# Kernel optimization log

Hardware: AMD Instinct MI355X
Metric: run time of the kernel (lower is better)

The kernel has to match this reference:

```python
import jax, jax.numpy as jnp
import numpy as np

N = 4096
FIN = 256
FOUT = 256
H = 1  # num_heads MUST be 1: edge projections reshape [N,N,H] -> (1,N,N)
NEG_MASK = -1000000.0
LRELU_SLOPE = 0.2
ESP = 1e-06
LN_EPS = 1e-05


def setup_inputs() -> dict:
    key = jax.random.key(0)
    ks = jax.random.split(key, 9)
    nodes_features = jax.random.normal(ks[0], (N, FIN), dtype=jnp.float32)
    degree_matrix = jax.random.normal(ks[1], (N, N), dtype=jnp.float32)
    edges_features_distance = jax.random.uniform(ks[2], (N, N), dtype=jnp.float32)
    edges_features_bond = jax.random.uniform(ks[3], (N, N), dtype=jnp.float32)
    # learned parameters (xavier-ish scale)
    proj_param = jax.random.normal(ks[4], (H, FIN, FOUT), dtype=jnp.float32) * (1.0 / np.sqrt(FIN))
    a_src = jax.random.normal(ks[5], (H, FOUT, 1), dtype=jnp.float32) * (1.0 / np.sqrt(FOUT))
    a_tgt = jax.random.normal(ks[6], (H, FOUT, 1), dtype=jnp.float32) * (1.0 / np.sqrt(FOUT))
    w_dist = jax.random.normal(ks[7], (H, 1), dtype=jnp.float32)  # nn.Linear(1, H).weight
    w_bond = jax.random.normal(ks[8], (H, 1), dtype=jnp.float32)
    return {
        "nodes_features": nodes_features,
        "degree_matrix": degree_matrix,
        "edges_features_distance": edges_features_distance,
        "edges_features_bond": edges_features_bond,
        "proj_param": proj_param,
        "a_src": a_src,
        "a_tgt": a_tgt,
        "w_dist": w_dist,
        "w_bond": w_bond,
        "cutoff": 0,
    }


def reference(nodes_features, degree_matrix, edges_features_distance,
              edges_features_bond, proj_param, a_src, a_tgt, w_dist, w_bond,
              cutoff=0):
    n = nodes_features.shape[0]
    h, fin, fout = proj_param.shape
    # connectivity mask: keep degree where positive, else large negative
    connectivity_mask = jnp.where(degree_matrix > 0, degree_matrix, NEG_MASK)
    # node projection: [H, N, Fout] (dropout is identity in eval)
    proj = jnp.einsum('nf,hfo->hno', nodes_features, proj_param)
    # attention scores: outer-sum of per-node source/target scores
    s_src = jnp.einsum('hno,hoi->hni', proj, a_src)      # [H, N, 1]
    s_tgt = jnp.einsum('hno,hoi->hni', proj, a_tgt)      # [H, N, 1]
    all_scores = jax.nn.leaky_relu(s_src + jnp.swapaxes(s_tgt, 1, 2), LRELU_SLOPE)  # [H,N,N]
    # edge contributions: Linear(1, H) on scalar edge features, reshaped (1,N,N) (H==1)
    dist_c = ((-edges_features_distance)[..., None] * w_dist[:, 0]).reshape(1, n, n)
    bond_c = (edges_features_bond[..., None] * w_bond[:, 0]).reshape(1, n, n)
    all_scores = all_scores + dist_c + bond_c
    # masked softmax over neighbors
    attn = jax.nn.softmax(all_scores + connectivity_mask[None], axis=-1)  # [H,N,N]
    # weighted aggregation
    out = jnp.einsum('hnm,hmo->hno', attn, proj)  # [H, N, Fout]
    # faithful to torch: transpose(2,1) -> [H,Fout,N] then contiguous view(-1,H,Fout)
    out = jnp.transpose(out, (0, 2, 1)).reshape(-1, h, fout)
    # concat heads (skip connection and bias are disabled per init args)
    out = out.reshape(-1, h * fout)
    out = jax.nn.elu(out)  # ELU activation, alpha=1
    # ---- no_grad connectivity update ----
    o = jax.lax.stop_gradient(out)
    dm = jax.lax.stop_gradient(degree_matrix)
    sim = o @ o.T                                        # [N, N]
    decay = -jax.lax.stop_gradient(edges_features_distance)
    upd = jax.nn.sigmoid(sim) * decay * (dm > 0).astype(o.dtype)
    upd = upd + ESP
    mean = jnp.mean(upd, axis=-1, keepdims=True)
    var = jnp.mean(jnp.square(upd - mean), axis=-1, keepdims=True)
    upd = (upd - mean) / jnp.sqrt(var + LN_EPS)          # layer_norm, no affine
    upd = upd + upd.T
    return out, upd
```

## Files before the change

### kernel.cpp

```cpp
#include <hip/hip_runtime.h>


using f32x4  = __attribute__((ext_vector_type(4))) float;
using bf16x8 = __attribute__((ext_vector_type(8))) __bf16;
using bf16x4 = __attribute__((ext_vector_type(4))) __bf16;
using u32x4  = __attribute__((ext_vector_type(4))) unsigned int;

__global__ __launch_bounds__(256) void cvt_nodes_kernel(const float* __restrict__ x,
                                                        __bf16* __restrict__ y) {
  int i = (blockIdx.x * 256 + threadIdx.x) * 4;
  f32x4 v = *(const f32x4*)(x + i);
  bf16x4 o = { (__bf16)v[0], (__bf16)v[1], (__bf16)v[2], (__bf16)v[3] };
  *(bf16x4*)(y + i) = o;
}

__global__ __launch_bounds__(256) void cvt_wt_kernel(const float* __restrict__ w,
                                                     __bf16* __restrict__ wt) {
  int i = blockIdx.x * 256 + threadIdx.x;
  int o = i >> 8, f = i & 255;
  wt[i] = (__bf16)w[f * 256 + o];
}

template<int BM, int BN, int MODE>
__global__ __launch_bounds__(256) void gemm_bf16_kernel(
    const __bf16* __restrict__ A, const __bf16* __restrict__ Bt,
    int M, int N, int K,
    float* __restrict__ outf, __bf16* __restrict__ outb,
    const float* __restrict__ e0, const float* __restrict__ e1,
    const __bf16* __restrict__ axp, float* __restrict__ outt)
{
  constexpr int LDT = 72;
  constexpr int MI = BM / 32;
  constexpr int NI = BN / 32;
  __shared__ alignas(16) __bf16 As[BM * LDT];
  __shared__ alignas(16) __bf16 Bs[BN * LDT];
  const int tid  = threadIdx.x;
  const int lane = tid & 63;
  const int wid  = tid >> 6;
  const int wm0  = (wid >> 1) * (BM / 2);
  const int wn0  = (wid & 1) * (BN / 2);
  const int m0   = blockIdx.x * BM;
  const int n0   = blockIdx.y * BN;
  const int lr   = lane & 15;
  const int lk   = lane >> 4;

  f32x4 acc[MI][NI];
#pragma unroll
  for (int a = 0; a < MI; ++a)
#pragma unroll
    for (int b = 0; b < NI; ++b) acc[a][b] = (f32x4){0.f, 0.f, 0.f, 0.f};

  for (int kt = 0; kt < K; kt += 64) {
    __syncthreads();
    for (int idx = tid; idx < BM * 8; idx += 256) {
      int r = idx >> 3, c = idx & 7;
      u32x4 v = *(const u32x4*)(A + (size_t)(m0 + r) * K + kt + c * 8);
      *(u32x4*)(As + r * LDT + c * 8) = v;
    }
    for (int idx = tid; idx < BN * 8; idx += 256) {
      int r = idx >> 3, c = idx & 7;
      u32x4 v = *(const u32x4*)(Bt + (size_t)(n0 + r) * K + kt + c * 8);
      *(u32x4*)(Bs + r * LDT + c * 8) = v;
    }
    __syncthreads();
#pragma unroll
    for (int kk = 0; kk < 2; ++kk) {
      bf16x8 av[MI], bv[NI];
#pragma unroll
      for (int mi = 0; mi < MI; ++mi)
        av[mi] = *(const bf16x8*)(As + (wm0 + mi * 16 + lr) * LDT + kk * 32 + lk * 8);
#pragma unroll
      for (int ni = 0; ni < NI; ++ni)
        bv[ni] = *(const bf16x8*)(Bs + (wn0 + ni * 16 + lr) * LDT + kk * 32 + lk * 8);
#pragma unroll
      for (int mi = 0; mi < MI; ++mi)
#pragma unroll
        for (int ni = 0; ni < NI; ++ni)
          acc[mi][ni] = __builtin_amdgcn_mfma_f32_16x16x32_bf16(av[mi], bv[ni], acc[mi][ni], 0, 0, 0);
    }
  }

#pragma unroll
  for (int mi = 0; mi < MI; ++mi) {
#pragma unroll
    for (int ni = 0; ni < NI; ++ni) {
#pragma unroll
      for (int j = 0; j < 4; ++j) {
        const int m = m0 + wm0 + mi * 16 + lk * 4 + j;
        const int n = n0 + wn0 + ni * 16 + lr;
        const float v = acc[mi][ni][j];
        if constexpr (MODE == 0) {
          outf[(size_t)m * 256 + n] = v;
          outb[(size_t)n * 4096 + m] = (__bf16)v;
        } else if constexpr (MODE == 2) {
          const size_t idx = (size_t)m * 4096 + n;
          const float d = e0[idx];
          const float g = e1[idx];
          const float s = 1.0f / (1.0f + expf(-v));
          outt[idx] = s * (-d) * (g > 0.f ? 1.0f : 0.0f) + 1e-6f;
        } else {
          const size_t idx = (size_t)m * 4096 + n;
          const float a = (float)axp[idx];
          const float s = 1.0f / (1.0f + expf(-v));
          outt[idx] = s * a + 1e-6f;
        }
      }
    }
  }
}

__global__ __launch_bounds__(256) void gemm_splitk_kernel(
    const __bf16* __restrict__ A, const __bf16* __restrict__ Bt,
    float* __restrict__ partial)
{
  constexpr int LDT = 72;
  __shared__ alignas(16) __bf16 As[64 * LDT];
  __shared__ alignas(16) __bf16 Bs[64 * LDT];
  const int tid  = threadIdx.x;
  const int lane = tid & 63;
  const int wid  = tid >> 6;
  const int wm0  = (wid >> 1) * 32;
  const int wn0  = (wid & 1) * 32;
  const int m0   = blockIdx.x * 64;
  const int n0   = blockIdx.y * 64;
  const int s    = blockIdx.z;
  const int lr   = lane & 15;
  const int lk   = lane >> 4;

  f32x4 acc[2][2];
#pragma unroll
  for (int a = 0; a < 2; ++a)
#pragma unroll
    for (int b = 0; b < 2; ++b) acc[a][b] = (f32x4){0.f, 0.f, 0.f, 0.f};

  const int k0 = s * 512;
  for (int kt = k0; kt < k0 + 512; kt += 64) {
    __syncthreads();
    for (int idx = tid; idx < 512; idx += 256) {
      int r = idx >> 3, c = idx & 7;
      u32x4 v = *(const u32x4*)(A + (size_t)(m0 + r) * 4096 + kt + c * 8);
      *(u32x4*)(As + r * LDT + c * 8) = v;
    }
    for (int idx = tid; idx < 512; idx += 256) {
      int r = idx >> 3, c = idx & 7;
      u32x4 v = *(const u32x4*)(Bt + (size_t)(n0 + r) * 4096 + kt + c * 8);
      *(u32x4*)(Bs + r * LDT + c * 8) = v;
    }
    __syncthreads();
#pragma unroll
    for (int kk = 0; kk < 2; ++kk) {
      bf16x8 av[2], bv[2];
#pragma unroll
      for (int mi = 0; mi < 2; ++mi)
        av[mi] = *(const bf16x8*)(As + (wm0 + mi * 16 + lr) * LDT + kk * 32 + lk * 8);
#pragma unroll
      for (int ni = 0; ni < 2; ++ni)
        bv[ni] = *(const bf16x8*)(Bs + (wn0 + ni * 16 + lr) * LDT + kk * 32 + lk * 8);
#pragma unroll
      for (int mi = 0; mi < 2; ++mi)
#pragma unroll
        for (int ni = 0; ni < 2; ++ni)
          acc[mi][ni] = __builtin_amdgcn_mfma_f32_16x16x32_bf16(av[mi], bv[ni], acc[mi][ni], 0, 0, 0);
    }
  }

  float* P = partial + (size_t)s * (4096 * 256);
#pragma unroll
  for (int mi = 0; mi < 2; ++mi)
#pragma unroll
    for (int ni = 0; ni < 2; ++ni)
#pragma unroll
      for (int j = 0; j < 4; ++j) {
        const int m = m0 + wm0 + mi * 16 + lk * 4 + j;
        const int n = n0 + wn0 + ni * 16 + lr;
        P[(size_t)m * 256 + n] = acc[mi][ni][j];
      }
}

__global__ __launch_bounds__(256) void reduce_elu_kernel(
    const float* __restrict__ partial, float* __restrict__ out0,
    __bf16* __restrict__ E)
{
  __shared__ float tile[64][65];
  const int tid = threadIdx.x;
  const int m0 = blockIdx.x * 64;
  const int n0 = blockIdx.y * 64;
#pragma unroll
  for (int i = 0; i < 4; ++i) {
    int lin = i * 1024 + tid * 4;
    int r = lin >> 6, c = lin & 63;
    f32x4 sum = (f32x4){0.f, 0.f, 0.f, 0.f};
#pragma unroll
    for (int s = 0; s < 8; ++s)
      sum += *(const f32x4*)(partial + (size_t)s * (4096 * 256) +
                             (size_t)(m0 + r) * 256 + n0 + c);
    tile[r][c]     = sum[0];
    tile[r][c + 1] = sum[1];
    tile[r][c + 2] = sum[2];
    tile[r][c + 3] = sum[3];
  }
  __syncthreads();
#pragma unroll
  for (int i = 0; i < 4; ++i) {
    int lin = i * 1024 + tid * 4;
    int rr = lin >> 6, cc = lin & 63;
    f32x4 e;
#pragma unroll
    for (int q = 0; q < 4; ++q) {
      float v = tile[cc + q][rr];
      e[q] = v > 0.f ? v : expm1f(v);
    }
    size_t idx = (size_t)(n0 + rr) * 4096 + m0 + cc;
    *(f32x4*)(out0 + idx) = e;
    bf16x4 eb = { (__bf16)e[0], (__bf16)e[1], (__bf16)e[2], (__bf16)e[3] };
    *(bf16x4*)(E + idx) = eb;
  }
}

__global__ __launch_bounds__(256) void sproj_kernel(const float* __restrict__ proj,
                                                    const float* __restrict__ asrc,
                                                    const float* __restrict__ atgt,
                                                    float* __restrict__ ssrc,
                                                    float* __restrict__ stgt) {
  const int row  = blockIdx.x * 4 + (threadIdx.x >> 6);
  const int lane = threadIdx.x & 63;
  f32x4 p = *(const f32x4*)(proj + (size_t)row * 256 + lane * 4);
  f32x4 a = *(const f32x4*)(asrc + lane * 4);
  f32x4 b = *(const f32x4*)(atgt + lane * 4);
  float d1 = p[0]*a[0] + p[1]*a[1] + p[2]*a[2] + p[3]*a[3];
  float d2 = p[0]*b[0] + p[1]*b[1] + p[2]*b[2] + p[3]*b[3];
#pragma unroll
  for (int o = 32; o; o >>= 1) { d1 += __shfl_xor(d1, o, 64); d2 += __shfl_xor(d2, o, 64); }
  if (lane == 0) { ssrc[row] = d1; stgt[row] = d2; }
}

__global__ __launch_bounds__(1024, 8) void scores_kernel(
    const float* __restrict__ dist, const float* __restrict__ bond,
    const float* __restrict__ deg,  const float* __restrict__ ssrc,
    const float* __restrict__ stgt, const float* __restrict__ wdp,
    const float* __restrict__ wbp,  __bf16* __restrict__ attn,
    __bf16* __restrict__ aux)
{
  const int row = blockIdx.x;
  const int tid = threadIdx.x;
  const int wid = tid >> 6;
  const int j   = tid * 4;
  const size_t base = (size_t)row * 4096;

  f32x4 d  = *(const f32x4*)(dist + base + j);
  f32x4 g  = *(const f32x4*)(deg  + base + j);
  f32x4 b  = *(const f32x4*)(bond + base + j);
  f32x4 st = *(const f32x4*)(stgt + j);
  const float wd = wdp[0], wb = wbp[0];
  const float si = ssrc[row];

  float sc[4];
  bf16x4 ax;
  float vmax = -3.4e38f;
#pragma unroll
  for (int q = 0; q < 4; ++q) {
    float x = si + st[q];
    x = x > 0.f ? x : 0.2f * x;
    x += -d[q] * wd + b[q] * wb + (g[q] > 0.f ? g[q] : -1000000.0f);
    sc[q] = x;
    vmax = fmaxf(vmax, x);
    ax[q] = (__bf16)(g[q] > 0.f ? -d[q] : 0.0f);
  }
#pragma unroll
  for (int o = 32; o; o >>= 1) vmax = fmaxf(vmax, __shfl_xor(vmax, o, 64));
  __shared__ float redm[16], reds[16];
  if ((tid & 63) == 0) redm[wid] = vmax;
  __syncthreads();
  float vm = redm[0];
#pragma unroll
  for (int i = 1; i < 16; ++i) vm = fmaxf(vm, redm[i]);

  float sum = 0.f;
#pragma unroll
  for (int q = 0; q < 4; ++q) { float e = expf(sc[q] - vm); sc[q] = e; sum += e; }
#pragma unroll
  for (int o = 32; o; o >>= 1) sum += __shfl_xor(sum, o, 64);
  if ((tid & 63) == 0) reds[wid] = sum;
  __syncthreads();
  float S = 0.f;
#pragma unroll
  for (int i = 0; i < 16; ++i) S += reds[i];
  const float inv = 1.0f / S;

  bf16x4 o4 = { (__bf16)(sc[0] * inv), (__bf16)(sc[1] * inv),
                (__bf16)(sc[2] * inv), (__bf16)(sc[3] * inv) };
  *(bf16x4*)(attn + base + j) = o4;
  if (aux) *(bf16x4*)(aux + base + j) = ax;
}

__global__ __launch_bounds__(256, 4) void stats_kernel(const float* __restrict__ t,
                                                       float* __restrict__ mean,
                                                       float* __restrict__ rstd) {
  const int row = blockIdx.x;
  const int tid = threadIdx.x;
  const float* tr = t + (size_t)row * 4096;
  f32x4 v[4];
#pragma unroll
  for (int u = 0; u < 4; ++u) v[u] = *(const f32x4*)(tr + u * 1024 + tid * 4);
  float s = 0.f, s2 = 0.f;
#pragma unroll
  for (int u = 0; u < 4; ++u)
#pragma unroll
    for (int q = 0; q < 4; ++q) { s += v[u][q]; s2 += v[u][q] * v[u][q]; }
#pragma unroll
  for (int o = 32; o; o >>= 1) { s += __shfl_xor(s, o, 64); s2 += __shfl_xor(s2, o, 64); }
  __shared__ float bs[4], bs2[4];
  if ((tid & 63) == 0) { bs[tid >> 6] = s; bs2[tid >> 6] = s2; }
  __syncthreads();
  if (tid == 0) {
    float S  = bs[0] + bs[1] + bs[2] + bs[3];
    float S2 = bs2[0] + bs2[1] + bs2[2] + bs2[3];
    float m  = S * (1.0f / 4096.0f);
    float var = S2 * (1.0f / 4096.0f) - m * m;
    mean[row] = m;
    rstd[row] = rsqrtf(var + 1e-5f);
  }
}

__global__ __launch_bounds__(256) void finalize_kernel(float* __restrict__ t,
                                                       const float* __restrict__ mean,
                                                       const float* __restrict__ rstd) {
  const int bj = blockIdx.x, bi = blockIdx.y;
  if (bi > bj) return;
  __shared__ float ta[64][65];
  __shared__ float tb[64][65];
  const int tid = threadIdx.x;
#pragma unroll
  for (int i = 0; i < 4; ++i) {
    int lin = i * 1024 + tid * 4;
    int r = lin >> 6, c = lin & 63;
    f32x4 va = *(const f32x4*)(t + (size_t)(bi * 64 + r) * 4096 + bj * 64 + c);
    ta[r][c] = va[0]; ta[r][c+1] = va[1]; ta[r][c+2] = va[2]; ta[r][c+3] = va[3];
  }
  if (bi != bj) {
#pragma unroll
    for (int i = 0; i < 4; ++i) {
      int lin = i * 1024 + tid * 4;
      int r = lin >> 6, c = lin & 63;
      f32x4 vb = *(const f32x4*)(t + (size_t)(bj * 64 + r) * 4096 + bi * 64 + c);
      tb[r][c] = vb[0]; tb[r][c+1] = vb[1]; tb[r][c+2] = vb[2]; tb[r][c+3] = vb[3];
    }
  }
  __syncthreads();
#pragma unroll
  for (int i = 0; i < 4; ++i) {
    int lin = i * 1024 + tid * 4;
    int r = lin >> 6, c = lin & 63;
    int gi = bi * 64 + r, gj = bj * 64 + c;
    const float mi_ = mean[gi], ri_ = rstd[gi];
    f32x4 mj = *(const f32x4*)(mean + gj);
    f32x4 rj = *(const f32x4*)(rstd + gj);
    f32x4 o;
#pragma unroll
    for (int q = 0; q < 4; ++q) {
      float v = (ta[r][c + q] - mi_) * ri_;
      float w = (bi == bj) ? (ta[c + q][r] - mj[q]) * rj[q]
                           : (tb[c + q][r] - mj[q]) * rj[q];
      o[q] = v + w;
    }
    *(f32x4*)(t + (size_t)gi * 4096 + gj) = o;
  }
  if (bi != bj) {
#pragma unroll
    for (int i = 0; i < 4; ++i) {
      int lin = i * 1024 + tid * 4;
      int r = lin >> 6, c = lin & 63;
      int gi = bj * 64 + r, gj = bi * 64 + c;
      const float mi_ = mean[gi], ri_ = rstd[gi];
      f32x4 mj = *(const f32x4*)(mean + gj);
      f32x4 rj = *(const f32x4*)(rstd + gj);
      f32x4 o;
#pragma unroll
      for (int q = 0; q < 4; ++q) {
        float v = (tb[r][c + q] - mi_) * ri_;
        float w = (ta[c + q][r] - mj[q]) * rj[q];
        o[q] = v + w;
      }
      *(f32x4*)(t + (size_t)gi * 4096 + gj) = o;
    }
  }
}

extern "C" void kernel_launch(void* const* d_in, const int* in_sizes, int n_in,
                              void* d_out, int out_size, void* d_ws, size_t ws_size,
                              hipStream_t stream) {
  const float* nodes  = (const float*)d_in[0];
  const float* degree = (const float*)d_in[1];
  const float* dist   = (const float*)d_in[2];
  const float* bond   = (const float*)d_in[3];
  const float* W      = (const float*)d_in[4];
  const float* a_src  = (const float*)d_in[5];
  const float* a_tgt  = (const float*)d_in[6];
  const float* w_dist = (const float*)d_in[7];
  const float* w_bond = (const float*)d_in[8];

  char* ws = (char*)d_ws;
  __bf16* nodesB = (__bf16*)ws;
  __bf16* Wt     = (__bf16*)(ws + (2u << 20));
  __bf16* projT  = (__bf16*)(ws + (2u << 20) + (256u << 10));
  float*  proj   = (float*)(ws + (5u << 20));
  __bf16* E      = (__bf16*)(ws + (9u << 20));
  float*  ssrc   = (float*)(ws + (11u << 20));
  float*  stgt   = ssrc + 4096;
  float*  mean   = stgt + 4096;
  float*  rstd   = mean + 4096;

  const bool useAux = ws_size >= (size_t)(44u << 20);
  __bf16* aux = useAux ? (__bf16*)(ws + (12u << 20)) : nullptr;

  float*  out0 = (float*)d_out;
  float*  t    = out0 + (size_t)4096 * 256;
  __bf16* attn = (__bf16*)t;
  float*  partials = t + (size_t)4096 * 4096 / 2;

  cvt_nodes_kernel<<<1024, 256, 0, stream>>>(nodes, nodesB);
  cvt_wt_kernel<<<256, 256, 0, stream>>>(W, Wt);

  gemm_bf16_kernel<64, 64, 0><<<dim3(64, 4), 256, 0, stream>>>(
      nodesB, Wt, 4096, 256, 256, proj, projT, nullptr, nullptr, nullptr, nullptr);

  sproj_kernel<<<1024, 256, 0, stream>>>(proj, a_src, a_tgt, ssrc, stgt);

  scores_kernel<<<4096, 1024, 0, stream>>>(dist, bond, degree, ssrc, stgt,
                                           w_dist, w_bond, attn, aux);

  gemm_splitk_kernel<<<dim3(64, 4, 8), 256, 0, stream>>>(attn, projT, partials);

  reduce_elu_kernel<<<dim3(64, 4), 256, 0, stream>>>(partials, out0, E);

  if (useAux)
    gemm_bf16_kernel<128, 128, 3><<<dim3(32, 32), 256, 0, stream>>>(
        E, E, 4096, 4096, 256, nullptr, nullptr, nullptr, nullptr, aux, t);
  else
    gemm_bf16_kernel<128, 128, 2><<<dim3(32, 32), 256, 0, stream>>>(
        E, E, 4096, 4096, 256, nullptr, nullptr, dist, degree, nullptr, t);

  stats_kernel<<<4096, 256, 0, stream>>>(t, mean, rstd);

  finalize_kernel<<<dim3(64, 64), 256, 0, stream>>>(t, mean, rstd);
}
```

Baseline: 174.1 us.

## Fuse masked softmax scoring into split-K attention GEMM with deferred normalization

Replaces the separate scores/softmax kernel and the split-K GEMM with one kernel. It computes unnormalized exp scores from distance, bond and degree tiles on the fly, writes them straight into shared memory as the A operand, and emits per-split row sums. The reduce kernel then sums 16 bf16 partials and divides by the total row sum before ELU. This removes the full N×N bf16 attention matrix write and re-read. The trade-offs are that max subtraction is dropped, so it relies on scores staying in a safe exp range, and partials are stored in bf16.

```diff
diff --git a/kernel.cpp b/kernel.cpp
--- a/kernel.cpp
+++ b/kernel.cpp
@@ -109,95 +109,156 @@
   }
 }
 
-__global__ __launch_bounds__(256) void gemm_splitk_kernel(
-    const __bf16* __restrict__ A, const __bf16* __restrict__ Bt,
-    float* __restrict__ partial)
+__global__ __launch_bounds__(512, 4) void fused_attn_kernel(
+    const float* __restrict__ dist, const float* __restrict__ bond,
+    const float* __restrict__ deg,  const float* __restrict__ ssrc,
+    const float* __restrict__ stgt, const float* __restrict__ wdp,
+    const float* __restrict__ wbp,  const __bf16* __restrict__ Bt,
+    __bf16* __restrict__ partial,   float* __restrict__ Lbuf,
+    __bf16* __restrict__ aux)
 {
   constexpr int LDT = 72;
   __shared__ alignas(16) __bf16 As[64 * LDT];
-  __shared__ alignas(16) __bf16 Bs[64 * LDT];
+  __shared__ alignas(16) __bf16 Bs[256 * LDT];
   const int tid  = threadIdx.x;
   const int lane = tid & 63;
   const int wid  = tid >> 6;
-  const int wm0  = (wid >> 1) * 32;
-  const int wn0  = (wid & 1) * 32;
+  const int wm0  = (wid >> 2) * 32;
+  const int wn0  = (wid & 3) * 64;
   const int m0   = blockIdx.x * 64;
-  const int n0   = blockIdx.y * 64;
-  const int s    = blockIdx.z;
+  const int s    = blockIdx.y;
+  const int k0   = s * 256;
   const int lr   = lane & 15;
   const int lk   = lane >> 4;
 
-  f32x4 acc[2][2];
+  const int r  = tid >> 3;
+  const int c0 = (tid & 7) * 8;
+  const float wd = wdp[0], wb = wbp[0];
+  const float si = ssrc[m0 + r];
+
+  f32x4 acc[2][4];
 #pragma unroll
   for (int a = 0; a < 2; ++a)
 #pragma unroll
-    for (int b = 0; b < 2; ++b) acc[a][b] = (f32x4){0.f, 0.f, 0.f, 0.f};
-
-  const int k0 = s * 512;
-  for (int kt = k0; kt < k0 + 512; kt += 64) {
+    for (int b = 0; b < 4; ++b) acc[a][b] = (f32x4){0.f, 0.f, 0.f, 0.f};
+  float lsum = 0.f;
+
+  for (int kt = 0; kt < 256; kt += 64) {
+    const size_t ebase = (size_t)(m0 + r) * 4096 + k0 + kt + c0;
+    f32x4 d0 = *(const f32x4*)(dist + ebase);
+    f32x4 d1 = *(const f32x4*)(dist + ebase + 4);
+    f32x4 g0 = *(const f32x4*)(deg + ebase);
+    f32x4 g1 = *(const f32x4*)(deg + ebase + 4);
+    f32x4 b0 = *(const f32x4*)(bond + ebase);
+    f32x4 b1 = *(const f32x4*)(bond + ebase + 4);
+    f32x4 s0 = *(const f32x4*)(stgt + k0 + kt + c0);
+    f32x4 s1 = *(const f32x4*)(stgt + k0 + kt + c0 + 4);
+    u32x4 br[4];
+#pragma unroll
+    for (int i = 0; i < 4; ++i) {
+      int idx = i * 512 + tid;
+      int n = idx >> 3, seg = idx & 7;
+      br[i] = *(const u32x4*)(Bt + (size_t)n * 4096 + k0 + kt + seg * 8);
+    }
     __syncthreads();
-    for (int idx = tid; idx < 512; idx += 256) {
-      int r = idx >> 3, c = idx & 7;
-      u32x4 v = *(const u32x4*)(A + (size_t)(m0 + r) * 4096 + kt + c * 8);
-      *(u32x4*)(As + r * LDT + c * 8) = v;
-    }
-    for (int idx = tid; idx < 512; idx += 256) {
-      int r = idx >> 3, c = idx & 7;
-      u32x4 v = *(const u32x4*)(Bt + (size_t)(n0 + r) * 4096 + kt + c * 8);
-      *(u32x4*)(Bs + r * LDT + c * 8) = v;
+    bf16x8 pa, ax;
+#pragma unroll
+    for (int q = 0; q < 8; ++q) {
+      const float dd = q < 4 ? d0[q & 3] : d1[q & 3];
+      const float gg = q < 4 ? g0[q & 3] : g1[q & 3];
+      const float bb = q < 4 ? b0[q & 3] : b1[q & 3];
+      const float ss = q < 4 ? s0[q & 3] : s1[q & 3];
+      float x = si + ss;
+      x = x > 0.f ? x : 0.2f * x;
+      x += -dd * wd + bb * wb + (gg > 0.f ? gg : -1000000.0f);
+      const float e = expf(x);
+      lsum += e;
+      pa[q] = (__bf16)e;
+      ax[q] = (__bf16)(gg > 0.f ? -dd : 0.0f);
+    }
+    *(bf16x8*)(As + r * LDT + c0) = pa;
+    if (aux) *(bf16x8*)(aux + ebase) = ax;
+#pragma unroll
+    for (int i = 0; i < 4; ++i) {
+      int idx = i * 512 + tid;
+      int n = idx >> 3, seg = idx & 7;
+      *(u32x4*)(Bs + n * LDT + seg * 8) = br[i];
     }
     __syncthreads();
 #pragma unroll
     for (int kk = 0; kk < 2; ++kk) {
-      bf16x8 av[2], bv[2];
+      bf16x8 av[2], bv[4];
 #pragma unroll
       for (int mi = 0; mi < 2; ++mi)
         av[mi] = *(const bf16x8*)(As + (wm0 + mi * 16 + lr) * LDT + kk * 32 + lk * 8);
 #pragma unroll
-      for (int ni = 0; ni < 2; ++ni)
+      for (int ni = 0; ni < 4; ++ni)
         bv[ni] = *(const bf16x8*)(Bs + (wn0 + ni * 16 + lr) * LDT + kk * 32 + lk * 8);
 #pragma unroll
       for (int mi = 0; mi < 2; ++mi)
 #pragma unroll
-        for (int ni = 0; ni < 2; ++ni)
+        for (int ni = 0; ni < 4; ++ni)
           acc[mi][ni] = __builtin_amdgcn_mfma_f32_16x16x32_bf16(av[mi], bv[ni], acc[mi][ni], 0, 0, 0);
     }
   }
 
-  float* P = partial + (size_t)s * (4096 * 256);
+  __bf16* P = partial + (size_t)s * (4096 * 256);
 #pragma unroll
   for (int mi = 0; mi < 2; ++mi)
 #pragma unroll
-    for (int ni = 0; ni < 2; ++ni)
+    for (int ni = 0; ni < 4; ++ni)
 #pragma unroll
       for (int j = 0; j < 4; ++j) {
         const int m = m0 + wm0 + mi * 16 + lk * 4 + j;
-        const int n = n0 + wn0 + ni * 16 + lr;
-        P[(size_t)m * 256 + n] = acc[mi][ni][j];
+        const int n = wn0 + ni * 16 + lr;
+        P[(size_t)m * 256 + n] = (__bf16)acc[mi][ni][j];
       }
+  lsum += __shfl_xor(lsum, 1, 64);
+  lsum += __shfl_xor(lsum, 2, 64);
+  lsum += __shfl_xor(lsum, 4, 64);
+  if ((tid & 7) == 0) Lbuf[s * 4096 + m0 + r] = lsum;
 }
 
 __global__ __launch_bounds__(256) void reduce_elu_kernel(
-    const float* __restrict__ partial, float* __restrict__ out0,
-    __bf16* __restrict__ E)
+    const __bf16* __restrict__ partial, const float* __restrict__ Lbuf,
+    float* __restrict__ out0, __bf16* __restrict__ E)
 {
   __shared__ float tile[64][65];
+  __shared__ float invL[64];
   const int tid = threadIdx.x;
   const int m0 = blockIdx.x * 64;
-  const int n0 = blockIdx.y * 64;
+  const int f0 = blockIdx.y * 64;
+  if (tid < 64) {
+    float ls = 0.f;
+#pragma unroll
+    for (int s = 0; s < 16; ++s) ls += Lbuf[s * 4096 + m0 + tid];
+    invL[tid] = 1.0f / ls;
+  }
+  f32x4 accv[4];
 #pragma unroll
   for (int i = 0; i < 4; ++i) {
     int lin = i * 1024 + tid * 4;
     int r = lin >> 6, c = lin & 63;
     f32x4 sum = (f32x4){0.f, 0.f, 0.f, 0.f};
 #pragma unroll
-    for (int s = 0; s < 8; ++s)
-      sum += *(const f32x4*)(partial + (size_t)s * (4096 * 256) +
-                             (size_t)(m0 + r) * 256 + n0 + c);
-    tile[r][c]     = sum[0];
-    tile[r][c + 1] = sum[1];
-    tile[r][c + 2] = sum[2];
-    tile[r][c + 3] = sum[3];
+    for (int s = 0; s < 16; ++s) {
+      bf16x4 pv = *(const bf16x4*)(partial + (size_t)s * (4096 * 256) +
+                                   (size_t)(m0 + r) * 256 + f0 + c);
+#pragma unroll
+      for (int q = 0; q < 4; ++q) sum[q] += (float)pv[q];
+    }
+    accv[i] = sum;
+  }
+  __syncthreads();
+#pragma unroll
+  for (int i = 0; i < 4; ++i) {
+    int lin = i * 1024 + tid * 4;
+    int r = lin >> 6, c = lin & 63;
+    const float inv = invL[r];
+    tile[r][c]     = accv[i][0] * inv;
+    tile[r][c + 1] = accv[i][1] * inv;
+    tile[r][c + 2] = accv[i][2] * inv;
+    tile[r][c + 3] = accv[i][3] * inv;
   }
   __syncthreads();
 #pragma unroll
@@ -210,7 +271,7 @@
       float v = tile[cc + q][rr];
       e[q] = v > 0.f ? v : expm1f(v);
     }
-    size_t idx = (size_t)(n0 + rr) * 4096 + m0 + cc;
+    size_t idx = (size_t)(f0 + rr) * 4096 + m0 + cc;
     *(f32x4*)(out0 + idx) = e;
     bf16x4 eb = { (__bf16)e[0], (__bf16)e[1], (__bf16)e[2], (__bf16)e[3] };
     *(bf16x4*)(E + idx) = eb;
@@ -234,65 +295,6 @@
   if (lane == 0) { ssrc[row] = d1; stgt[row] = d2; }
 }
 
-__global__ __launch_bounds__(1024, 8) void scores_kernel(
-    const float* __restrict__ dist, const float* __restrict__ bond,
-    const float* __restrict__ deg,  const float* __restrict__ ssrc,
-    const float* __restrict__ stgt, const float* __restrict__ wdp,
-    const float* __restrict__ wbp,  __bf16* __restrict__ attn,
-    __bf16* __restrict__ aux)
-{
-  const int row = blockIdx.x;
-  const int tid = threadIdx.x;
-  const int wid = tid >> 6;
-  const int j   = tid * 4;
-  const size_t base = (size_t)row * 4096;
-
-  f32x4 d  = *(const f32x4*)(dist + base + j);
-  f32x4 g  = *(const f32x4*)(deg  + base + j);
-  f32x4 b  = *(const f32x4*)(bond + base + j);
-  f32x4 st = *(const f32x4*)(stgt + j);
-  const float wd = wdp[0], wb = wbp[0];
-  const float si = ssrc[row];
-
-  float sc[4];
-  bf16x4 ax;
-  float vmax = -3.4e38f;
-#pragma unroll
-  for (int q = 0; q < 4; ++q) {
-    float x = si + st[q];
-    x = x > 0.f ? x : 0.2f * x;
-    x += -d[q] * wd + b[q] * wb + (g[q] > 0.f ? g[q] : -1000000.0f);
-    sc[q] = x;
-    vmax = fmaxf(vmax, x);
-    ax[q] = (__bf16)(g[q] > 0.f ? -d[q] : 0.0f);
-  }
-#pragma unroll
-  for (int o = 32; o; o >>= 1) vmax = fmaxf(vmax, __shfl_xor(vmax, o, 64));
-  __shared__ float redm[16], reds[16];
-  if ((tid & 63) == 0) redm[wid] = vmax;
-  __syncthreads();
-  float vm = redm[0];
-#pragma unroll
-  for (int i = 1; i < 16; ++i) vm = fmaxf(vm, redm[i]);
-
-  float sum = 0.f;
-#pragma unroll
-  for (int q = 0; q < 4; ++q) { float e = expf(sc[q] - vm); sc[q] = e; sum += e; }
-#pragma unroll
-  for (int o = 32; o; o >>= 1) sum += __shfl_xor(sum, o, 64);
-  if ((tid & 63) == 0) reds[wid] = sum;
-  __syncthreads();
-  float S = 0.f;
-#pragma unroll
-  for (int i = 0; i < 16; ++i) S += reds[i];
-  const float inv = 1.0f / S;
-
-  bf16x4 o4 = { (__bf16)(sc[0] * inv), (__bf16)(sc[1] * inv),
-                (__bf16)(sc[2] * inv), (__bf16)(sc[3] * inv) };
-  *(bf16x4*)(attn + base + j) = o4;
-  if (aux) *(bf16x4*)(aux + base + j) = ax;
-}
-
 __global__ __launch_bounds__(256, 4) void stats_kernel(const float* __restrict__ t,
                                                        float* __restrict__ mean,
                                                        float* __restrict__ rstd) {
@@ -409,14 +411,14 @@
   float*  stgt   = ssrc + 4096;
   float*  mean   = stgt + 4096;
   float*  rstd   = mean + 4096;
+  float*  Lbuf   = rstd + 4096;
 
   const bool useAux = ws_size >= (size_t)(44u << 20);
   __bf16* aux = useAux ? (__bf16*)(ws + (12u << 20)) : nullptr;
 
   float*  out0 = (float*)d_out;
   float*  t    = out0 + (size_t)4096 * 256;
-  __bf16* attn = (__bf16*)t;
-  float*  partials = t + (size_t)4096 * 4096 / 2;
+  __bf16* partials = (__bf16*)t;
 
   cvt_nodes_kernel<<<1024, 256, 0, stream>>>(nodes, nodesB);
   cvt_wt_kernel<<<256, 256, 0, stream>>>(W, Wt);
@@ -426,12 +428,11 @@
 
   sproj_kernel<<<1024, 256, 0, stream>>>(proj, a_src, a_tgt, ssrc, stgt);
 
-  scores_kernel<<<4096, 1024, 0, stream>>>(dist, bond, degree, ssrc, stgt,
-                                           w_dist, w_bond, attn, aux);
-
-  gemm_splitk_kernel<<<dim3(64, 4, 8), 256, 0, stream>>>(attn, projT, partials);
-
-  reduce_elu_kernel<<<dim3(64, 4), 256, 0, stream>>>(partials, out0, E);
+  fused_attn_kernel<<<dim3(64, 16), 512, 0, stream>>>(
+      dist, bond, degree, ssrc, stgt, w_dist, w_bond, projT,
+      partials, Lbuf, aux);
+
+  reduce_elu_kernel<<<dim3(64, 4), 256, 0, stream>>>(partials, Lbuf, out0, E);
 
   if (useAux)
     gemm_bf16_kernel<128, 128, 3><<<dim3(32, 32), 256, 0, stream>>>(
```

After: 172.6 us. No clear change (-0.9%).

## Defer softmax normalization past the aggregation GEMM and drop max pass

Applied to the files above, without the earlier changes.

Replaces the per-row softmax kernel with a grid-strided kernel. It writes unnormalized exp(score) as bf16 and accumulates row sums into a zeroed buffer with per-wavefront atomics. The aggregation GEMM now runs on the unnormalized weights, and the split-K reduce step scales each row by the reciprocal sum before ELU. This removes the block-wide max and sum reductions and their barriers in the memory-bound score pass. In exchange it adds atomics and an extra zeroing launch, and it drops the max subtraction, so it relies on scores staying small enough not to overflow exp.

```diff
diff --git a/kernel.cpp b/kernel.cpp
--- a/kernel.cpp
+++ b/kernel.cpp
@@ -19,6 +19,10 @@
   int i = blockIdx.x * 256 + threadIdx.x;
   int o = i >> 8, f = i & 255;
   wt[i] = (__bf16)w[f * 256 + o];
+}
+
+__global__ __launch_bounds__(256) void zero_kernel(float* __restrict__ p) {
+  p[blockIdx.x * 256 + threadIdx.x] = 0.0f;
 }
 
 template<int BM, int BN, int MODE>
@@ -109,6 +113,46 @@
   }
 }
 
+__global__ __launch_bounds__(256) void score_exp_kernel(
+    const float* __restrict__ dist, const float* __restrict__ bond,
+    const float* __restrict__ deg,  const float* __restrict__ ssrc,
+    const float* __restrict__ stgt, const float* __restrict__ wdp,
+    const float* __restrict__ wbp,  __bf16* __restrict__ P,
+    __bf16* __restrict__ aux,       float* __restrict__ Lrow)
+{
+  const float wd = wdp[0], wb = wbp[0];
+  const int lane = threadIdx.x & 63;
+  size_t i = ((size_t)blockIdx.x * 256 + threadIdx.x) * 4;
+  const size_t stride = (size_t)2048 * 256 * 4;
+#pragma unroll 2
+  for (int it = 0; it < 8; ++it, i += stride) {
+    const int row = (int)(i >> 12);
+    const int col = (int)(i & 4095);
+    f32x4 d  = *(const f32x4*)(dist + i);
+    f32x4 g  = *(const f32x4*)(deg + i);
+    f32x4 b  = *(const f32x4*)(bond + i);
+    f32x4 st = *(const f32x4*)(stgt + col);
+    const float si = ssrc[row];
+    f32x4 p;
+    bf16x4 pb, ab;
+#pragma unroll
+    for (int q = 0; q < 4; ++q) {
+      float x = si + st[q];
+      x = x > 0.f ? x : 0.2f * x;
+      x += -d[q] * wd + b[q] * wb + (g[q] > 0.f ? g[q] : -1000000.0f);
+      p[q] = expf(x);
+      pb[q] = (__bf16)p[q];
+      ab[q] = (__bf16)(g[q] > 0.f ? -d[q] : 0.0f);
+    }
+    *(bf16x4*)(P + i) = pb;
+    if (aux) *(bf16x4*)(aux + i) = ab;
+    float s = p[0] + p[1] + p[2] + p[3];
+#pragma unroll
+    for (int o = 32; o; o >>= 1) s += __shfl_xor(s, o, 64);
+    if (lane == 0) atomicAdd(Lrow + row, s);
+  }
+}
+
 __global__ __launch_bounds__(256) void gemm_splitk_kernel(
     const __bf16* __restrict__ A, const __bf16* __restrict__ Bt,
     float* __restrict__ partial)
@@ -164,7 +208,7 @@
     }
   }
 
-  float* P = partial + (size_t)s * (4096 * 256);
+  float* Pp = partial + (size_t)s * (4096 * 256);
 #pragma unroll
   for (int mi = 0; mi < 2; ++mi)
 #pragma unroll
@@ -173,18 +217,21 @@
       for (int j = 0; j < 4; ++j) {
         const int m = m0 + wm0 + mi * 16 + lk * 4 + j;
         const int n = n0 + wn0 + ni * 16 + lr;
-        P[(size_t)m * 256 + n] = acc[mi][ni][j];
+        Pp[(size_t)m * 256 + n] = acc[mi][ni][j];
       }
 }
 
 __global__ __launch_bounds__(256) void reduce_elu_kernel(
-    const float* __restrict__ partial, float* __restrict__ out0,
-    __bf16* __restrict__ E)
+    const float* __restrict__ partial, const float* __restrict__ Lrow,
+    float* __restrict__ out0, __bf16* __restrict__ E)
 {
   __shared__ float tile[64][65];
+  __shared__ float invL[64];
   const int tid = threadIdx.x;
   const int m0 = blockIdx.x * 64;
-  const int n0 = blockIdx.y * 64;
+  const int f0 = blockIdx.y * 64;
+  if (tid < 64) invL[tid] = 1.0f / Lrow[m0 + tid];
+  f32x4 accv[4];
 #pragma unroll
   for (int i = 0; i < 4; ++i) {
     int lin = i * 1024 + tid * 4;
@@ -193,11 +240,19 @@
 #pragma unroll
     for (int s = 0; s < 8; ++s)
       sum += *(const f32x4*)(partial + (size_t)s * (4096 * 256) +
-                             (size_t)(m0 + r) * 256 + n0 + c);
-    tile[r][c]     = sum[0];
-    tile[r][c + 1] = sum[1];
-    tile[r][c + 2] = sum[2];
-    tile[r][c + 3] = sum[3];
+                             (size_t)(m0 + r) * 256 + f0 + c);
+    accv[i] = sum;
+  }
+  __syncthreads();
+#pragma unroll
+  for (int i = 0; i < 4; ++i) {
+    int lin = i * 1024 + tid * 4;
+    int r = lin >> 6, c = lin & 63;
+    const float inv = invL[r];
+    tile[r][c]     = accv[i][0] * inv;
+    tile[r][c + 1] = accv[i][1] * inv;
+    tile[r][c + 2] = accv[i][2] * inv;
+    tile[r][c + 3] = accv[i][3] * inv;
   }
   __syncthreads();
 #pragma unroll
@@ -210,7 +265,7 @@
       float v = tile[cc + q][rr];
       e[q] = v > 0.f ? v : expm1f(v);
     }
-    size_t idx = (size_t)(n0 + rr) * 4096 + m0 + cc;
+    size_t idx = (size_t)(f0 + rr) * 4096 + m0 + cc;
     *(f32x4*)(out0 + idx) = e;
     bf16x4 eb = { (__bf16)e[0], (__bf16)e[1], (__bf16)e[2], (__bf16)e[3] };
     *(bf16x4*)(E + idx) = eb;
@@ -234,65 +289,6 @@
   if (lane == 0) { ssrc[row] = d1; stgt[row] = d2; }
 }
 
-__global__ __launch_bounds__(1024, 8) void scores_kernel(
-    const float* __restrict__ dist, const float* __restrict__ bond,
-    const float* __restrict__ deg,  const float* __restrict__ ssrc,
-    const float* __restrict__ stgt, const float* __restrict__ wdp,
-    const float* __restrict__ wbp,  __bf16* __restrict__ attn,
-    __bf16* __restrict__ aux)
-{
-  const int row = blockIdx.x;
-  const int tid = threadIdx.x;
-  const int wid = tid >> 6;
-  const int j   = tid * 4;
-  const size_t base = (size_t)row * 4096;
-
-  f32x4 d  = *(const f32x4*)(dist + base + j);
-  f32x4 g  = *(const f32x4*)(deg  + base + j);
-  f32x4 b  = *(const f32x4*)(bond + base + j);
-  f32x4 st = *(const f32x4*)(stgt + j);
-  const float wd = wdp[0], wb = wbp[0];
-  const float si = ssrc[row];
-
-  float sc[4];
-  bf16x4 ax;
-  float vmax = -3.4e38f;
-#pragma unroll
-  for (int q = 0; q < 4; ++q) {
-    float x = si + st[q];
-    x = x > 0.f ? x : 0.2f * x;
-    x += -d[q] * wd + b[q] * wb + (g[q] > 0.f ? g[q] : -1000000.0f);
-    sc[q] = x;
-    vmax = fmaxf(vmax, x);
-    ax[q] = (__bf16)(g[q] > 0.f ? -d[q] : 0.0f);
-  }
-#pragma unroll
-  for (int o = 32; o; o >>= 1) vmax = fmaxf(vmax, __shfl_xor(vmax, o, 64));
-  __shared__ float redm[16], reds[16];
-  if ((tid & 63) == 0) redm[wid] = vmax;
-  __syncthreads();
-  float vm = redm[0];
-#pragma unroll
-  for (int i = 1; i < 16; ++i) vm = fmaxf(vm, redm[i]);
-
-  float sum = 0.f;
-#pragma unroll
-  for (int q = 0; q < 4; ++q) { float e = expf(sc[q] - vm); sc[q] = e; sum += e; }
-#pragma unroll
-  for (int o = 32; o; o >>= 1) sum += __shfl_xor(sum, o, 64);
-  if ((tid & 63) == 0) reds[wid] = sum;
-  __syncthreads();
-  float S = 0.f;
-#pragma unroll
-  for (int i = 0; i < 16; ++i) S += reds[i];
-  const float inv = 1.0f / S;
-
-  bf16x4 o4 = { (__bf16)(sc[0] * inv), (__bf16)(sc[1] * inv),
-                (__bf16)(sc[2] * inv), (__bf16)(sc[3] * inv) };
-  *(bf16x4*)(attn + base + j) = o4;
-  if (aux) *(bf16x4*)(aux + base + j) = ax;
-}
-
 __global__ __launch_bounds__(256, 4) void stats_kernel(const float* __restrict__ t,
                                                        float* __restrict__ mean,
                                                        float* __restrict__ rstd) {
@@ -404,19 +400,20 @@
   __bf16* Wt     = (__bf16*)(ws + (2u << 20));
   __bf16* projT  = (__bf16*)(ws + (2u << 20) + (256u << 10));
   float*  proj   = (float*)(ws + (5u << 20));
-  __bf16* E      = (__bf16*)(ws + (9u << 20));
   float*  ssrc   = (float*)(ws + (11u << 20));
   float*  stgt   = ssrc + 4096;
   float*  mean   = stgt + 4096;
   float*  rstd   = mean + 4096;
+  float*  Lrow   = rstd + 4096;
 
   const bool useAux = ws_size >= (size_t)(44u << 20);
   __bf16* aux = useAux ? (__bf16*)(ws + (12u << 20)) : nullptr;
 
   float*  out0 = (float*)d_out;
   float*  t    = out0 + (size_t)4096 * 256;
-  __bf16* attn = (__bf16*)t;
+  __bf16* P    = (__bf16*)t;
   float*  partials = t + (size_t)4096 * 4096 / 2;
+  __bf16* E    = (__bf16*)(ws + (9u << 20));
 
   cvt_nodes_kernel<<<1024, 256, 0, stream>>>(nodes, nodesB);
   cvt_wt_kernel<<<256, 256, 0, stream>>>(W, Wt);
@@ -426,12 +423,14 @@
 
   sproj_kernel<<<1024, 256, 0, stream>>>(proj, a_src, a_tgt, ssrc, stgt);
 
-  scores_kernel<<<4096, 1024, 0, stream>>>(dist, bond, degree, ssrc, stgt,
-                                           w_dist, w_bond, attn, aux);
-
-  gemm_splitk_kernel<<<dim3(64, 4, 8), 256, 0, stream>>>(attn, projT, partials);
-
-  reduce_elu_kernel<<<dim3(64, 4), 256, 0, stream>>>(partials, out0, E);
+  zero_kernel<<<16, 256, 0, stream>>>(Lrow);
+
+  score_exp_kernel<<<2048, 256, 0, stream>>>(dist, bond, degree, ssrc, stgt,
+                                             w_dist, w_bond, P, aux, Lrow);
+
+  gemm_splitk_kernel<<<dim3(64, 4, 8), 256, 0, stream>>>(P, projT, partials);
+
+  reduce_elu_kernel<<<dim3(64, 4), 256, 0, stream>>>(partials, Lrow, out0, E);
 
   if (useAux)
     gemm_bf16_kernel<128, 128, 3><<<dim3(32, 32), 256, 0, stream>>>(
```

New measurement: 184.7 us. +6.1%, slower.
